# Kernel tuning notes

Measured on AMD Instinct MI355X. Metric: run time of the kernel, lower is better.

## Reference

```python
import jax, jax.numpy as jnp
import numpy as np

N = 50000   # nodes
E = 640000  # edges
D = 128     # feature dim


def setup_inputs() -> dict:
    key = jax.random.key(0)
    k1, k2, k3, k4 = jax.random.split(key, 4)
    feat = jax.random.normal(k1, (N, D), dtype=jnp.float32)
    edge_weight = jax.random.normal(k2, (E,), dtype=jnp.float32)
    src = jax.random.randint(k3, (E,), 0, N)
    dst = jax.random.randint(k4, (E,), 0, N)
    beta = jnp.ones((1,), dtype=jnp.float32)   # learn_beta=True -> init 1
    eps = jnp.zeros((1,), dtype=jnp.float32)   # initial_eps = 0.0
    return {"feat": feat, "edge_weight": edge_weight, "src": src,
            "dst": dst, "beta": beta, "eps": eps}


def reference(feat, edge_weight, src, dst, beta, eps):
    n = feat.shape[0]
    # F.normalize(feat, p=2, dim=-1) with eps clamp
    norm = jnp.linalg.norm(feat, axis=-1, keepdims=True)
    norm_h = feat / jnp.maximum(norm, 1e-12)
    # e = beta * edge_weight, edge softmax grouped by SOURCE node (norm_by='src')
    e = beta[0] * edge_weight                               # [E]
    seg_max = jax.ops.segment_max(e, src, num_segments=n)   # [N]
    ex = jnp.exp(e - seg_max[src])                          # [E]
    seg_sum = jax.ops.segment_sum(ex, src, num_segments=n)  # [N]
    p = ex / seg_sum[src]                                   # [E]
    # message: u_mul_e(norm_h, p); reduce: sum at dst
    msg = norm_h[src] * p[:, None]                          # [E, D]
    h = jax.ops.segment_sum(msg, dst, num_segments=n)       # [N, D]
    return (1.0 + eps[0]) * feat + h
```

## Files before the change

### kernel.cpp

```cpp
#include <hip/hip_runtime.h>
#include <hip/hip_bf16.h>
#include <math.h>

#define FD 128
#define CAP 48
#define BSH 7
#define BINW 128
#define NBMAX 512
#define BCAP 2048
#define P2_BS 512
#define P2_K 8
#define P2_EPB 4096

typedef float v2f __attribute__((ext_vector_type(2)));

__device__ __forceinline__ float bf2f(unsigned u) { return __uint_as_float(u << 16); }
__device__ __forceinline__ unsigned f2bf(float f) {
    return (unsigned)__bfloat16_as_ushort(__float2bfloat16(f));
}

__device__ __forceinline__ int excl_scan512(int cnt, int t, int* wsum) {
    int lane = t & 63, wv = t >> 6;
    int x = cnt;
    #pragma unroll
    for (int d = 1; d < 64; d <<= 1) {
        int y = __shfl_up(x, d, 64);
        if (lane >= d) x += y;
    }
    if (lane == 63) wsum[wv] = x;
    __syncthreads();
    if (t == 0) {
        int a = 0;
        #pragma unroll
        for (int j = 0; j < 8; ++j) { int tp = wsum[j]; wsum[j] = a; a += tp; }
    }
    __syncthreads();
    return x - cnt + wsum[wv];
}

__global__ void __launch_bounds__(P2_BS) k_all(
        const float* __restrict__ ew, const int* __restrict__ src,
        const int* __restrict__ dst, const float* __restrict__ beta,
        const float* __restrict__ feat,
        int* __restrict__ cur_src, int* __restrict__ cur_dst,
        unsigned* __restrict__ reg_src,
        unsigned long long* __restrict__ reg_dst,
        unsigned short* __restrict__ f8,
        int e, int n, int sg) {
    __shared__ unsigned long long smem[P2_EPB];
    __shared__ int h_cnt[NBMAX], h_base[NBMAX], h_rank[NBMAX], h_gbase[NBMAX];
    __shared__ int wsum[8];
    int b = blockIdx.x, t = threadIdx.x;

    if (b < sg) {
        unsigned* buf = (unsigned*)smem;
        h_cnt[t] = 0; h_rank[t] = 0;
        __syncthreads();
        int base0 = b * P2_EPB;
        float bb = beta[0];
        unsigned pay[P2_K]; int bn[P2_K];
        #pragma unroll
        for (int k = 0; k < P2_K; ++k) {
            int i = base0 + k * P2_BS + t;
            if (i < e) {
                int s = src[i];
                pay[k] = ((unsigned)s << 16) | f2bf(__expf(bb * ew[i]));
                bn[k] = s >> BSH;
                atomicAdd(&h_cnt[bn[k]], 1);
            } else bn[k] = -1;
        }
        __syncthreads();
        int cnt = h_cnt[t];
        int excl = excl_scan512(cnt, t, wsum);
        h_base[t] = excl;
        if (cnt > 0) h_gbase[t] = atomicAdd(&cur_src[t], cnt);
        __syncthreads();
        #pragma unroll
        for (int k = 0; k < P2_K; ++k) {
            if (bn[k] >= 0) {
                int r = atomicAdd(&h_rank[bn[k]], 1);
                buf[h_base[bn[k]] + r] = pay[k];
            }
        }
        __syncthreads();
        int tot = min(e - base0, P2_EPB);
        for (int p = t; p < tot; p += P2_BS) {
            unsigned q = buf[p];
            int b2 = (int)(q >> 16) >> BSH;
            int pos = h_gbase[b2] + (p - h_base[b2]);
            if (pos < BCAP) reg_src[(size_t)b2 * BCAP + pos] = q;
        }
    } else if (b < 2 * sg) {
        unsigned long long* buf = smem;
        h_cnt[t] = 0; h_rank[t] = 0;
        __syncthreads();
        int base0 = (b - sg) * P2_EPB;
        float bb = beta[0];
        unsigned long long pay[P2_K]; int bn[P2_K];
        #pragma unroll
        for (int k = 0; k < P2_K; ++k) {
            int i = base0 + k * P2_BS + t;
            if (i < e) {
                int s = src[i], d = dst[i];
                float ex = __expf(bb * ew[i]);
                pay[k] = ((unsigned long long)__float_as_uint(ex) << 32)
                       | ((unsigned long long)(unsigned)s << 16) | (unsigned)d;
                bn[k] = d >> BSH;
                atomicAdd(&h_cnt[bn[k]], 1);
            } else bn[k] = -1;
        }
        __syncthreads();
        int cnt = h_cnt[t];
        int excl = excl_scan512(cnt, t, wsum);
        h_base[t] = excl;
        if (cnt > 0) h_gbase[t] = atomicAdd(&cur_dst[t], cnt);
        __syncthreads();
        #pragma unroll
        for (int k = 0; k < P2_K; ++k) {
            if (bn[k] >= 0) {
                int r = atomicAdd(&h_rank[bn[k]], 1);
                buf[h_base[bn[k]] + r] = pay[k];
            }
        }
        __syncthreads();
        int tot = min(e - base0, P2_EPB);
        for (int p = t; p < tot; p += P2_BS) {
            unsigned long long qq = buf[p];
            int b2 = (int)(qq & 0xffffULL) >> BSH;
            int pos = h_gbase[b2] + (p - h_base[b2]);
            if (pos < BCAP) reg_dst[(size_t)b2 * BCAP + pos] = qq;
        }
    } else {
        int row  = (b - 2 * sg) * (P2_BS >> 6) + (t >> 6);
        int lane = t & 63;
        if (row >= n) return;
        float2 v = reinterpret_cast<const float2*>(feat + (size_t)row * FD)[lane];
        float s = v.x * v.x + v.y * v.y;
        #pragma unroll
        for (int m = 32; m >= 1; m >>= 1) s += __shfl_xor(s, m, 64);
        float inv = 1.0f / fmaxf(sqrtf(s), 1e-12f);
        unsigned pk = __builtin_amdgcn_cvt_pk_fp8_f32(v.x * inv, v.y * inv, 0, false);
        f8[(size_t)row * 64 + lane] = (unsigned short)(pk & 0xffffu);
    }
}

__global__ void __launch_bounds__(P2_BS) k_seg_reduce(
        const int* __restrict__ cur_src,
        const unsigned* __restrict__ reg_src,
        float* __restrict__ rcp_seg, int n) {
    __shared__ float acc[BINW];
    int b = blockIdx.x, t = threadIdx.x;
    if (t < BINW) acc[t] = 0.0f;
    __syncthreads();
    int cnt = min(cur_src[b], BCAP);
    const unsigned* base = reg_src + (size_t)b * BCAP;
    for (int i = t; i < cnt; i += P2_BS) {
        unsigned p = base[i];
        atomicAdd(&acc[(p >> 16) & (BINW - 1)], bf2f(p & 0xffffu));
    }
    __syncthreads();
    int row = b * BINW + t;
    if (t < BINW && row < n)
        rcp_seg[row] = 1.0f / acc[t];
}

__global__ void __launch_bounds__(512) k_gather(
        const float* __restrict__ feat,
        const unsigned short* __restrict__ f8,
        const float* __restrict__ rcp_seg,
        const int* __restrict__ cur_dst,
        const unsigned long long* __restrict__ reg_dst,
        const float* __restrict__ eps,
        float* __restrict__ out, int n) {
    __shared__ unsigned lp[64 * CAP];
    __shared__ int lc[64];
    int hb = blockIdx.x;
    int b = hb >> 1, half = hb & 1;
    int t = threadIdx.x;
    if (t < 64) lc[t] = 0;
    __syncthreads();
    int cnt_all = min(cur_dst[b], BCAP);
    const unsigned long long* base = reg_dst + (size_t)b * BCAP;
    for (int i = t; i < cnt_all; i += 512) {
        unsigned long long qq = base[i];
        int dl = (int)(qq & (unsigned long long)(BINW - 1));
        if ((dl >> 6) == half) {
            unsigned sv  = (unsigned)((qq >> 16) & 0xffffULL);
            unsigned exb = f2bf(__uint_as_float((unsigned)(qq >> 32)));
            int slot = atomicAdd(&lc[dl & 63], 1);
            if (slot < CAP) lp[(dl & 63) * CAP + slot] = (sv << 16) | exb;
        }
    }
    __syncthreads();
    int wv = t >> 6, lane = t & 63, q = lane >> 4, li = lane & 15;
    float c0 = 1.0f + eps[0];
    for (int rr = 0; rr < 8; ++rr) {
        int r = wv * 8 + rr;
        int row = b * BINW + half * 64 + r;
        if (row >= n) break;
        int cnt = min(lc[r], CAP);
        float acc[8];
        #pragma unroll
        for (int i = 0; i < 8; ++i) acc[i] = 0.0f;
        if (q == 0) {
            float4 f0 = reinterpret_cast<const float4*>(feat + (size_t)row * FD)[li * 2];
            float4 f1 = reinterpret_cast<const float4*>(feat + (size_t)row * FD)[li * 2 + 1];
            acc[0] = c0 * f0.x; acc[1] = c0 * f0.y; acc[2] = c0 * f0.z; acc[3] = c0 * f0.w;
            acc[4] = c0 * f1.x; acc[5] = c0 * f1.y; acc[6] = c0 * f1.z; acc[7] = c0 * f1.w;
        }
        int sv = 0; float cv = 0.0f;
        if (lane < cnt) {
            unsigned pr = lp[r * CAP + lane];
            sv = (int)(pr >> 16);
            cv = bf2f(pr & 0xffffu) * rcp_seg[sv];
        }
        for (int j = 0; j < cnt; j += 4) {
            int idx = j + q;
            int   ss = __shfl(sv, idx, 64);
            float cc = __shfl(cv, idx, 64);
            if (idx < cnt) {
                uint2 w = reinterpret_cast<const uint2*>(f8 + (size_t)ss * 64)[li];
                v2f p0 = __builtin_amdgcn_cvt_pk_f32_fp8(w.x, false);
                v2f p1 = __builtin_amdgcn_cvt_pk_f32_fp8(w.x, true);
                v2f p2 = __builtin_amdgcn_cvt_pk_f32_fp8(w.y, false);
                v2f p3 = __builtin_amdgcn_cvt_pk_f32_fp8(w.y, true);
                acc[0] = fmaf(cc, p0.x, acc[0]);
                acc[1] = fmaf(cc, p0.y, acc[1]);
                acc[2] = fmaf(cc, p1.x, acc[2]);
                acc[3] = fmaf(cc, p1.y, acc[3]);
                acc[4] = fmaf(cc, p2.x, acc[4]);
                acc[5] = fmaf(cc, p2.y, acc[5]);
                acc[6] = fmaf(cc, p3.x, acc[6]);
                acc[7] = fmaf(cc, p3.y, acc[7]);
            }
        }
        #pragma unroll
        for (int i = 0; i < 8; ++i) {
            acc[i] += __shfl_xor(acc[i], 16, 64);
            acc[i] += __shfl_xor(acc[i], 32, 64);
        }
        if (q == 0) {
            float4* orow = reinterpret_cast<float4*>(out + (size_t)row * FD);
            orow[li * 2]     = make_float4(acc[0], acc[1], acc[2], acc[3]);
            orow[li * 2 + 1] = make_float4(acc[4], acc[5], acc[6], acc[7]);
        }
    }
}


__global__ void k_fused(const float* __restrict__ ew, const int* __restrict__ src,
                        const int* __restrict__ dst, const float* __restrict__ beta,
                        const float* __restrict__ feat, float* __restrict__ seg_sum,
                        int* __restrict__ cursor, unsigned* __restrict__ pairs,
                        unsigned* __restrict__ fb16, int cap, int e, int n, int eb) {
    int b = blockIdx.x;
    if (b < eb) {
        int base = (b * blockDim.x + threadIdx.x) * 4;
        if (base >= e) return;
        float bb = beta[0];
        if (base + 4 <= e) {
            int4   s4 = *reinterpret_cast<const int4*>(src + base);
            int4   d4 = *reinterpret_cast<const int4*>(dst + base);
            float4 w4 = *reinterpret_cast<const float4*>(ew + base);
            float ex0 = __expf(bb * w4.x), ex1 = __expf(bb * w4.y);
            float ex2 = __expf(bb * w4.z), ex3 = __expf(bb * w4.w);
            unsafeAtomicAdd(&seg_sum[s4.x], ex0);
            unsafeAtomicAdd(&seg_sum[s4.y], ex1);
            unsafeAtomicAdd(&seg_sum[s4.z], ex2);
            unsafeAtomicAdd(&seg_sum[s4.w], ex3);
            int sl0 = atomicAdd(&cursor[d4.x], 1);
            int sl1 = atomicAdd(&cursor[d4.y], 1);
            int sl2 = atomicAdd(&cursor[d4.z], 1);
            int sl3 = atomicAdd(&cursor[d4.w], 1);
            if (sl0 < cap) pairs[(size_t)d4.x * cap + sl0] = ((unsigned)s4.x << 16) | f2bf(ex0);
            if (sl1 < cap) pairs[(size_t)d4.y * cap + sl1] = ((unsigned)s4.y << 16) | f2bf(ex1);
            if (sl2 < cap) pairs[(size_t)d4.z * cap + sl2] = ((unsigned)s4.z << 16) | f2bf(ex2);
            if (sl3 < cap) pairs[(size_t)d4.w * cap + sl3] = ((unsigned)s4.w << 16) | f2bf(ex3);
        } else {
            for (int i = base; i < e; ++i) {
                int s = src[i], d = dst[i];
                float ex = __expf(bb * ew[i]);
                unsafeAtomicAdd(&seg_sum[s], ex);
                int slot = atomicAdd(&cursor[d], 1);
                if (slot < cap) pairs[(size_t)d * cap + slot] = ((unsigned)s << 16) | f2bf(ex);
            }
        }
    } else {
        int row  = (b - eb) * (blockDim.x >> 6) + (threadIdx.x >> 6);
        int lane = threadIdx.x & 63;
        if (row >= n) return;
        float2 v = reinterpret_cast<const float2*>(feat + (size_t)row * FD)[lane];
        float s = v.x * v.x + v.y * v.y;
        #pragma unroll
        for (int m = 32; m >= 1; m >>= 1) s += __shfl_xor(s, m, 64);
        float inv = 1.0f / fmaxf(sqrtf(s), 1e-12f);
        fb16[(size_t)row * 64 + lane] = (f2bf(v.y * inv) << 16) | f2bf(v.x * inv);
    }
}

__global__ void __launch_bounds__(256) k_gather_p(
        const float* __restrict__ feat, const unsigned* __restrict__ fb16,
        const float* __restrict__ seg_sum, const int* __restrict__ cursor,
        const unsigned* __restrict__ pairs, const float* __restrict__ eps,
        float* __restrict__ out, int cap, int n) {
    int row  = blockIdx.x * (blockDim.x >> 6) + (threadIdx.x >> 6);
    int lane = threadIdx.x & 63;
    if (row >= n) return;
    int q = lane >> 4, li = lane & 15;
    int cnt = min(cursor[row], cap);
    float acc[8];
    #pragma unroll
    for (int i = 0; i < 8; ++i) acc[i] = 0.0f;
    if (q == 0) {
        float c0 = 1.0f + eps[0];
        float4 f0 = reinterpret_cast<const float4*>(feat + (size_t)row * FD)[li * 2];
        float4 f1 = reinterpret_cast<const float4*>(feat + (size_t)row * FD)[li * 2 + 1];
        acc[0] = c0 * f0.x; acc[1] = c0 * f0.y; acc[2] = c0 * f0.z; acc[3] = c0 * f0.w;
        acc[4] = c0 * f1.x; acc[5] = c0 * f1.y; acc[6] = c0 * f1.z; acc[7] = c0 * f1.w;
    }
    size_t beg = (size_t)row * cap;
    for (int k = 0; k < cnt; k += 64) {
        int m = min(64, cnt - k);
        int sv = 0; float cv = 0.0f;
        if (lane < m) {
            unsigned pr = pairs[beg + k + lane];
            sv = (int)(pr >> 16);
            cv = bf2f(pr & 0xffffu) / seg_sum[sv];
        }
        for (int j = 0; j < m; j += 4) {
            int idx = j + q;
            int   ss = __shfl(sv, idx, 64);
            float cc = __shfl(cv, idx, 64);
            if (idx < m) {
                uint4 w = reinterpret_cast<const uint4*>(fb16 + (size_t)ss * 64)[li];
                acc[0] = fmaf(cc, bf2f(w.x & 0xffffu), acc[0]);
                acc[1] = fmaf(cc, bf2f(w.x >> 16),     acc[1]);
                acc[2] = fmaf(cc, bf2f(w.y & 0xffffu), acc[2]);
                acc[3] = fmaf(cc, bf2f(w.y >> 16),     acc[3]);
                acc[4] = fmaf(cc, bf2f(w.z & 0xffffu), acc[4]);
                acc[5] = fmaf(cc, bf2f(w.z >> 16),     acc[5]);
                acc[6] = fmaf(cc, bf2f(w.w & 0xffffu), acc[6]);
                acc[7] = fmaf(cc, bf2f(w.w >> 16),     acc[7]);
            }
        }
    }
    #pragma unroll
    for (int i = 0; i < 8; ++i) {
        acc[i] += __shfl_xor(acc[i], 16, 64);
        acc[i] += __shfl_xor(acc[i], 32, 64);
    }
    if (q == 0) {
        float4* orow = reinterpret_cast<float4*>(out + (size_t)row * FD);
        orow[li * 2]     = make_float4(acc[0], acc[1], acc[2], acc[3]);
        orow[li * 2 + 1] = make_float4(acc[4], acc[5], acc[6], acc[7]);
    }
}


extern "C" void kernel_launch(void* const* d_in, const int* in_sizes, int n_in,
                              void* d_out, int out_size, void* d_ws, size_t ws_size,
                              hipStream_t stream) {
    const float* feat = (const float*)d_in[0];
    const float* ew   = (const float*)d_in[1];
    const int*   src  = (const int*)d_in[2];
    const int*   dst  = (const int*)d_in[3];
    const float* beta = (const float*)d_in[4];
    const float* eps  = (const float*)d_in[5];
    float* out = (float*)d_out;

    const int n = in_sizes[0] / FD;
    const int e = in_sizes[1];

    const int nb = (n + BINW - 1) >> BSH;

    size_t need_bin = (size_t)nb * BCAP * 8 + (size_t)nb * BCAP * 4 + (size_t)n * 4
                    + (size_t)(2 * nb) * 4 + (size_t)n * FD;

    if (n <= 65535 && nb <= NBMAX && ws_size >= need_bin) {
        unsigned long long* reg_dst = (unsigned long long*)d_ws;
        unsigned* reg_src = (unsigned*)(reg_dst + (size_t)nb * BCAP);
        float*    rcp_seg = (float*)(reg_src + (size_t)nb * BCAP);
        int*      cur_src = (int*)(rcp_seg + n);
        int*      cur_dst = cur_src + nb;
        unsigned short* f8 = (unsigned short*)(cur_dst + nb);

        hipMemsetAsync(cur_src, 0, (size_t)(2 * nb) * 4, stream);
        int sg = (e + P2_EPB - 1) / P2_EPB;
        int sb = (n + (P2_BS / 64) - 1) / (P2_BS / 64);
        k_all<<<2 * sg + sb, P2_BS, 0, stream>>>(ew, src, dst, beta, feat,
                                                 cur_src, cur_dst, reg_src, reg_dst,
                                                 f8, e, n, sg);
        k_seg_reduce<<<nb, P2_BS, 0, stream>>>(cur_src, reg_src, rcp_seg, n);
        k_gather<<<2 * nb, 512, 0, stream>>>(feat, f8, rcp_seg, cur_dst, reg_dst,
                                             eps, out, n);
    } else {
        const int rpb   = 256 / 64;
        const int ngrid = (n + rpb - 1) / rpb;
        const int eb    = ((e + 3) / 4 + 255) / 256;
        size_t fixed  = (size_t)n * 4 * 2;
        size_t fb16_b = (size_t)n * FD * 2;
        int cap = (ws_size >= (size_t)n * 64 * 4 + fixed + fb16_b) ? 64 : 48;

        unsigned* pairs   = (unsigned*)d_ws;
        float*    seg_sum = (float*)(pairs + (size_t)n * cap);
        int*      cursor  = (int*)(seg_sum + n);
        unsigned* fb16    = (unsigned*)(cursor + n);

        hipMemsetAsync(seg_sum, 0, fixed, stream);
        k_fused<<<eb + ngrid, 256, 0, stream>>>(ew, src, dst, beta, feat,
                                                seg_sum, cursor, pairs, fb16,
                                                cap, e, n, eb);
        k_gather_p<<<ngrid, 256, 0, stream>>>(feat, fb16, seg_sum, cursor, pairs,
                                              eps, out, cap, n);
    }
}
```

Measured before the change: 66.22 us.

## Merge src and dst binning into one block pass sharing edge loads

Before, separate blocks binned edges by source and by destination, and each set of blocks loaded the edge data and computed exp on its own. Now each block loads src, dst and edge weight once, computes exp once, then runs the src binning and the dst binning one after the other through the same shared buffer. Edges per block drop from 4096 to 2048, so the edge-block count stays the same while the number of global loads and exp evaluations falls. The cost is more barriers per block and a longer serial chain inside each block.

```diff
diff --git a/kernel.cpp b/kernel.cpp
--- a/kernel.cpp
+++ b/kernel.cpp
@@ -9,8 +9,8 @@
 #define NBMAX 512
 #define BCAP 2048
 #define P2_BS 512
-#define P2_K 8
-#define P2_EPB 4096
+#define MS_K 4
+#define MS_EPB 2048
 
 typedef float v2f __attribute__((ext_vector_type(2)));
 
@@ -47,91 +47,90 @@
         unsigned long long* __restrict__ reg_dst,
         unsigned short* __restrict__ f8,
         int e, int n, int sg) {
-    __shared__ unsigned long long smem[P2_EPB];
+    __shared__ unsigned long long smem[MS_EPB];
     __shared__ int h_cnt[NBMAX], h_base[NBMAX], h_rank[NBMAX], h_gbase[NBMAX];
     __shared__ int wsum[8];
     int b = blockIdx.x, t = threadIdx.x;
 
     if (b < sg) {
-        unsigned* buf = (unsigned*)smem;
-        h_cnt[t] = 0; h_rank[t] = 0;
-        __syncthreads();
-        int base0 = b * P2_EPB;
+        int base0 = b * MS_EPB;
         float bb = beta[0];
-        unsigned pay[P2_K]; int bn[P2_K];
-        #pragma unroll
-        for (int k = 0; k < P2_K; ++k) {
+        int   sv[MS_K], dv[MS_K];
+        float exv[MS_K];
+        #pragma unroll
+        for (int k = 0; k < MS_K; ++k) {
             int i = base0 + k * P2_BS + t;
             if (i < e) {
-                int s = src[i];
-                pay[k] = ((unsigned)s << 16) | f2bf(__expf(bb * ew[i]));
-                bn[k] = s >> BSH;
-                atomicAdd(&h_cnt[bn[k]], 1);
-            } else bn[k] = -1;
-        }
-        __syncthreads();
-        int cnt = h_cnt[t];
-        int excl = excl_scan512(cnt, t, wsum);
-        h_base[t] = excl;
-        if (cnt > 0) h_gbase[t] = atomicAdd(&cur_src[t], cnt);
-        __syncthreads();
-        #pragma unroll
-        for (int k = 0; k < P2_K; ++k) {
-            if (bn[k] >= 0) {
-                int r = atomicAdd(&h_rank[bn[k]], 1);
-                buf[h_base[bn[k]] + r] = pay[k];
-            }
-        }
-        __syncthreads();
-        int tot = min(e - base0, P2_EPB);
-        for (int p = t; p < tot; p += P2_BS) {
-            unsigned q = buf[p];
-            int b2 = (int)(q >> 16) >> BSH;
-            int pos = h_gbase[b2] + (p - h_base[b2]);
-            if (pos < BCAP) reg_src[(size_t)b2 * BCAP + pos] = q;
-        }
-    } else if (b < 2 * sg) {
-        unsigned long long* buf = smem;
-        h_cnt[t] = 0; h_rank[t] = 0;
-        __syncthreads();
-        int base0 = (b - sg) * P2_EPB;
-        float bb = beta[0];
-        unsigned long long pay[P2_K]; int bn[P2_K];
-        #pragma unroll
-        for (int k = 0; k < P2_K; ++k) {
-            int i = base0 + k * P2_BS + t;
-            if (i < e) {
-                int s = src[i], d = dst[i];
-                float ex = __expf(bb * ew[i]);
-                pay[k] = ((unsigned long long)__float_as_uint(ex) << 32)
-                       | ((unsigned long long)(unsigned)s << 16) | (unsigned)d;
-                bn[k] = d >> BSH;
-                atomicAdd(&h_cnt[bn[k]], 1);
-            } else bn[k] = -1;
-        }
-        __syncthreads();
-        int cnt = h_cnt[t];
-        int excl = excl_scan512(cnt, t, wsum);
-        h_base[t] = excl;
-        if (cnt > 0) h_gbase[t] = atomicAdd(&cur_dst[t], cnt);
-        __syncthreads();
-        #pragma unroll
-        for (int k = 0; k < P2_K; ++k) {
-            if (bn[k] >= 0) {
-                int r = atomicAdd(&h_rank[bn[k]], 1);
-                buf[h_base[bn[k]] + r] = pay[k];
-            }
-        }
-        __syncthreads();
-        int tot = min(e - base0, P2_EPB);
-        for (int p = t; p < tot; p += P2_BS) {
-            unsigned long long qq = buf[p];
-            int b2 = (int)(qq & 0xffffULL) >> BSH;
-            int pos = h_gbase[b2] + (p - h_base[b2]);
-            if (pos < BCAP) reg_dst[(size_t)b2 * BCAP + pos] = qq;
+                sv[k] = src[i];
+                dv[k] = dst[i];
+                exv[k] = __expf(bb * ew[i]);
+            } else sv[k] = -1;
+        }
+        {
+            unsigned* buf = (unsigned*)smem;
+            h_cnt[t] = 0; h_rank[t] = 0;
+            __syncthreads();
+            #pragma unroll
+            for (int k = 0; k < MS_K; ++k)
+                if (sv[k] >= 0) atomicAdd(&h_cnt[sv[k] >> BSH], 1);
+            __syncthreads();
+            int cnt = h_cnt[t];
+            int excl = excl_scan512(cnt, t, wsum);
+            h_base[t] = excl;
+            if (cnt > 0) h_gbase[t] = atomicAdd(&cur_src[t], cnt);
+            __syncthreads();
+            #pragma unroll
+            for (int k = 0; k < MS_K; ++k) {
+                if (sv[k] >= 0) {
+                    int bn = sv[k] >> BSH;
+                    int r = atomicAdd(&h_rank[bn], 1);
+                    buf[h_base[bn] + r] = ((unsigned)sv[k] << 16) | f2bf(exv[k]);
+                }
+            }
+            __syncthreads();
+            int tot = min(e - base0, MS_EPB);
+            for (int p = t; p < tot; p += P2_BS) {
+                unsigned q = buf[p];
+                int b2 = (int)(q >> 16) >> BSH;
+                int pos = h_gbase[b2] + (p - h_base[b2]);
+                if (pos < BCAP) reg_src[(size_t)b2 * BCAP + pos] = q;
+            }
+            __syncthreads();
+        }
+        {
+            unsigned long long* buf = smem;
+            h_cnt[t] = 0; h_rank[t] = 0;
+            __syncthreads();
+            #pragma unroll
+            for (int k = 0; k < MS_K; ++k)
+                if (sv[k] >= 0) atomicAdd(&h_cnt[dv[k] >> BSH], 1);
+            __syncthreads();
+            int cnt = h_cnt[t];
+            int excl = excl_scan512(cnt, t, wsum);
+            h_base[t] = excl;
+            if (cnt > 0) h_gbase[t] = atomicAdd(&cur_dst[t], cnt);
+            __syncthreads();
+            #pragma unroll
+            for (int k = 0; k < MS_K; ++k) {
+                if (sv[k] >= 0) {
+                    int bn = dv[k] >> BSH;
+                    int r = atomicAdd(&h_rank[bn], 1);
+                    buf[h_base[bn] + r] =
+                        ((unsigned long long)__float_as_uint(exv[k]) << 32)
+                      | ((unsigned long long)(unsigned)sv[k] << 16) | (unsigned)dv[k];
+                }
+            }
+            __syncthreads();
+            int tot = min(e - base0, MS_EPB);
+            for (int p = t; p < tot; p += P2_BS) {
+                unsigned long long qq = buf[p];
+                int b2 = (int)(qq & 0xffffULL) >> BSH;
+                int pos = h_gbase[b2] + (p - h_base[b2]);
+                if (pos < BCAP) reg_dst[(size_t)b2 * BCAP + pos] = qq;
+            }
         }
     } else {
-        int row  = (b - 2 * sg) * (P2_BS >> 6) + (t >> 6);
+        int row  = (b - sg) * (P2_BS >> 6) + (t >> 6);
         int lane = t & 63;
         if (row >= n) return;
         float2 v = reinterpret_cast<const float2*>(feat + (size_t)row * FD)[lane];
@@ -385,11 +384,11 @@
         unsigned short* f8 = (unsigned short*)(cur_dst + nb);
 
         hipMemsetAsync(cur_src, 0, (size_t)(2 * nb) * 4, stream);
-        int sg = (e + P2_EPB - 1) / P2_EPB;
+        int sg = (e + MS_EPB - 1) / MS_EPB;
         int sb = (n + (P2_BS / 64) - 1) / (P2_BS / 64);
-        k_all<<<2 * sg + sb, P2_BS, 0, stream>>>(ew, src, dst, beta, feat,
-                                                 cur_src, cur_dst, reg_src, reg_dst,
-                                                 f8, e, n, sg);
+        k_all<<<sg + sb, P2_BS, 0, stream>>>(ew, src, dst, beta, feat,
+                                             cur_src, cur_dst, reg_src, reg_dst,
+                                             f8, e, n, sg);
         k_seg_reduce<<<nb, P2_BS, 0, stream>>>(cur_src, reg_src, rcp_seg, n);
         k_gather<<<2 * nb, 512, 0, stream>>>(feat, f8, rcp_seg, cur_dst, reg_dst,
                                              eps, out, n);
```

Result: slower. 72.11 us (+8.9%).
